# Kernel optimization log

Hardware: AMD Instinct MI355X
Metric: run time of the kernel (lower is better)

The kernel has to match this reference:

```python
import jax, jax.numpy as jnp
import numpy as np
from functools import partial

N = 10  # n_qubits (static)


def _rx(state, w, theta, n):
    # state: [B, 2^n] complex64; RX(theta) on wire w (wire 0 = most significant)
    B = state.shape[0]
    st = state.reshape(B, 2 ** w, 2, 2 ** (n - 1 - w))
    half = jnp.asarray(theta, state.real.dtype) * 0.5
    c = jnp.cos(half).reshape(-1, 1, 1)
    s = jnp.sin(half).reshape(-1, 1, 1)
    s0, s1 = st[:, :, 0], st[:, :, 1]
    n0 = c * s0 - 1j * s * s1
    n1 = -1j * s * s0 + c * s1
    return jnp.stack([n0, n1], axis=2).reshape(B, 2 ** n)


def _cnot(state, control, target, n):
    B = state.shape[0]
    a, bb = (control, target) if control < target else (target, control)
    st = state.reshape(B, 2 ** a, 2, 2 ** (bb - a - 1), 2, 2 ** (n - 1 - bb))
    if control == a:
        # control is axis 2, target axis 4: flip target where control==1
        c1 = jnp.flip(st[:, :, 1], axis=3)
        st = jnp.stack([st[:, :, 0], c1], axis=2)
    else:
        # control is axis 4, target axis 2: flip axis-2 slice where control==1
        c1 = jnp.flip(st[:, :, :, :, 1], axis=1)
        st = jnp.stack([st[:, :, :, :, 0], c1], axis=4)
    return st.reshape(B, 2 ** n)


def _expect_z(state, n):
    B = state.shape[0]
    probs = jnp.abs(state) ** 2  # [B, 2^n]
    es = []
    for w in range(n):
        p = probs.reshape(B, 2 ** w, 2, 2 ** (n - 1 - w))
        es.append(p[:, :, 0].sum((1, 2)) - p[:, :, 1].sum((1, 2)))
    return jnp.stack(es, axis=1)  # [B, n]


def _qlayer(x, theta, n):
    # x: [B, n] encoder angles; theta: [n] trainable RX angles
    B = x.shape[0]
    state = jnp.zeros((B, 2 ** n), jnp.complex64).at[:, 0].set(1.0)
    for w in range(n):
        state = _rx(state, w, x[:, w], n)
    for w in range(n):
        state = _rx(state, w, theta[w], n)
    for w in range(n - 1):
        state = _cnot(state, w, w + 1, n)
    state = _cnot(state, n - 1, 0, n)
    return _expect_z(state, n)


def setup_inputs() -> dict:
    key = jax.random.key(0)
    k1, k2, k3, k4 = jax.random.split(key, 4)
    T, B, D, H = 64, 256, 246, N
    inputs = jax.random.normal(k1, (T, B, D), jnp.float32)
    fan_in = D + H
    W = jax.random.normal(k2, (4, N, fan_in), jnp.float32) / np.sqrt(fan_in)
    b = jax.random.normal(k3, (4, N), jnp.float32) * 0.01
    thetas = jax.random.normal(k4, (4, N), jnp.float32)
    return {"inputs": inputs, "W": W, "b": b, "thetas": thetas}


def reference(inputs, W, b, thetas):
    T, B, D = inputs.shape
    H = thetas.shape[-1]
    qlayer4 = jax.vmap(partial(_qlayer, n=N))  # over the 4 gates

    def step(carry, x_t):
        hx, cx = carry
        comb = jnp.concatenate([x_t, hx], axis=1)          # [B, D+H]
        z = jnp.einsum('bi,goi->gbo', comb, W) + b[:, None, :]  # [4, B, n]
        gates = qlayer4(z, thetas)                          # [4, B, n]
        f = jax.nn.sigmoid(gates[0])
        i = jax.nn.sigmoid(gates[1])
        g = jnp.tanh(gates[2])
        o = jax.nn.sigmoid(gates[3])
        cx = f * cx + i * g
        hx = o * jnp.tanh(cx)
        return (hx, cx), hx

    hx0 = jnp.zeros((B, H), inputs.dtype)
    cx0 = jnp.zeros((B, H), inputs.dtype)
    (hx, cx), outputs = jax.lax.scan(step, (hx0, cx0), inputs)
    return outputs, hx, cx
```

## Files before the change

kernel.cpp:

```cpp
#include <hip/hip_runtime.h>
#include <hip/hip_bf16.h>

#define D_IN   246
#define NW     10
#define NG     4
#define NOUT   40
#define FANIN  256
#define BATCH  256
#define TSTEPS 64
#define XP     248
#define WP_ELEMS (NG * D_IN * 16)

__global__ __launch_bounds__(256) void k_wt(const float* __restrict__ W,
                                            float* __restrict__ Wp) {
    int e = blockIdx.x * 256 + threadIdx.x;
    if (e >= WP_ELEMS) return;
    int o = e & 15;
    int i = (e >> 4) % D_IN;
    int g = e / (16 * D_IN);
    float v = (o < NW) ? W[(g * NW + o) * FANIN + i] : 0.f;
    Wp[e] = v;
}

__global__ __launch_bounds__(256) void k_zx(
    const float* __restrict__ x,
    const float* __restrict__ Wp,
    const float* __restrict__ bias,
    const float* __restrict__ theta,
    float* __restrict__ zxT)
{
    const int t   = blockIdx.x;
    const int bq  = blockIdx.y;
    const int tid = threadIdx.x;
    const int lane = tid & 63;
    const int g = __builtin_amdgcn_readfirstlane(tid >> 6);

    __shared__ float xl[64 * XP];

    const float* xsrc = x + ((size_t)t * BATCH + bq * 64) * D_IN;
    for (int k = tid; k < 64 * 123; k += 256) {
        int row = k / 123;
        int j   = k - row * 123;
        float2 v = *reinterpret_cast<const float2*>(xsrc + row * D_IN + 2 * j);
        *reinterpret_cast<float2*>(xl + row * XP + 2 * j) = v;
    }
    __syncthreads();

    float acc[NW];
#pragma unroll
    for (int o = 0; o < NW; ++o)
        acc[o] = bias[g * NW + o] + theta[g * NW + o];

    const float* wg = Wp + g * D_IN * 16;
    const float* xr = xl + lane * XP;

#pragma unroll 1
    for (int i = 0; i < 244; i += 4) {
        float4 xv = *reinterpret_cast<const float4*>(xr + i);
        const float xs[4] = {xv.x, xv.y, xv.z, xv.w};
#pragma unroll
        for (int k2 = 0; k2 < 4; ++k2) {
#pragma unroll
            for (int o = 0; o < NW; ++o)
                acc[o] += xs[k2] * wg[(i + k2) * 16 + o];
        }
    }
    {
        float2 xv = *reinterpret_cast<const float2*>(xr + 244);
#pragma unroll
        for (int o = 0; o < NW; ++o) {
            acc[o] += xv.x * wg[244 * 16 + o];
            acc[o] += xv.y * wg[245 * 16 + o];
        }
    }

    const int b = bq * 64 + lane;
    float* zo = zxT + ((size_t)b * TSTEPS + t) * NOUT + g * NW;
#pragma unroll
    for (int o = 0; o < NW; ++o) zo[o] = acc[o];
}

template <int CTRL>
__device__ __forceinline__ float dpp_shr_mul(float p) {
    int up = __builtin_amdgcn_update_dpp(__float_as_int(1.0f), __float_as_int(p),
                                         CTRL, 0xF, 0xF, false);
    return p * __int_as_float(up);
}

__global__ __launch_bounds__(64) void k_scan(
    const float* __restrict__ zxT,
    const float* __restrict__ W,
    float* __restrict__ out,
    float* __restrict__ hxout,
    float* __restrict__ cxout)
{
    const int b    = blockIdx.x;
    const int lane = threadIdx.x;
    const int r    = lane >> 4;
    const int o    = lane & 15;
    const bool act = (o < NW);
    const int oc   = act ? o : 0;

    __shared__ float zl[TSTEPS * NOUT];

    {
        const float4* src4 = reinterpret_cast<const float4*>(zxT + (size_t)b * TSTEPS * NOUT);
        float4* dst4 = reinterpret_cast<float4*>(zl);
#pragma unroll
        for (int q = 0; q < 10; ++q) dst4[q * 64 + lane] = src4[q * 64 + lane];
    }

    float wh[NW];
#pragma unroll
    for (int j = 0; j < NW; ++j)
        wh[j] = W[(r * NW + oc) * FANIN + D_IN + j];

    __syncthreads();

    float hx_s[NW];
#pragma unroll
    for (int j = 0; j < NW; ++j) hx_s[j] = 0.f;

    float cx = 0.f, hv = 0.f;
    const int cidx = r * NW + oc;
    float zc = act ? zl[cidx] : 0.f;

    for (int t = 0; t < TSTEPS; ++t) {
        float zn = (act && t < TSTEPS - 1) ? zl[(t + 1) * NOUT + cidx] : 0.f;

        float z = zc;
#pragma unroll
        for (int j = 0; j < NW; ++j) z += hx_s[j] * wh[j];

        float cv = act ? __cosf(z) : 1.0f;

        float p = cv;
        p = dpp_shr_mul<0x111>(p);
        p = dpp_shr_mul<0x112>(p);
        p = dpp_shr_mul<0x114>(p);
        p = dpp_shr_mul<0x118>(p);

        float a   = (r == 2) ? p + p : p;
        float sg  = __fdividef(1.f, 1.f + __expf(-a));
        float val = (r == 2) ? 2.f * sg - 1.f : sg;

        float v1 = __shfl(val, 16 + o);
        float v2 = __shfl(val, 32 + o);
        float v3 = __shfl(val, 48 + o);

        cx = val * cx + v1 * v2;
        float e2 = __expf(cx + cx);
        float th = 1.f - __fdividef(2.f, e2 + 1.f);
        hv = v3 * th;

        if (r == 0 && act) out[((size_t)t * BATCH + b) * NW + o] = hv;

#pragma unroll
        for (int j = 0; j < NW; ++j)
            hx_s[j] = __int_as_float(__builtin_amdgcn_readlane(__float_as_int(hv), j));

        zc = zn;
    }

    if (r == 0 && act) {
        hxout[b * NW + o] = hv;
        cxout[b * NW + o] = cx;
    }
}

extern "C" void kernel_launch(void* const* d_in, const int* in_sizes, int n_in,
                              void* d_out, int out_size, void* d_ws, size_t ws_size,
                              hipStream_t stream) {
    const float* x     = (const float*)d_in[0];
    const float* W     = (const float*)d_in[1];
    const float* bias  = (const float*)d_in[2];
    const float* theta = (const float*)d_in[3];

    float* out   = (float*)d_out;
    float* hxout = out + (size_t)TSTEPS * BATCH * NW;
    float* cxout = hxout + (size_t)BATCH * NW;

    float* Wp  = (float*)d_ws;
    float* zxT = Wp + WP_ELEMS;

    k_wt<<<(WP_ELEMS + 255) / 256, 256, 0, stream>>>(W, Wp);
    dim3 g1(TSTEPS, 4);
    k_zx<<<g1, 256, 0, stream>>>(x, Wp, bias, theta, zxT);
    k_scan<<<BATCH, 64, 0, stream>>>(zxT, W, out, hxout, cxout);
}
```

Before: 126.2 us.

## Split zx projection K-dimension across two waves and streamline scan step

The input-projection kernel now uses 512 threads, with each gate split into two half-K waves that reduce through shared memory, and it writes its outputs as float2 stores. The scan loop drops the active-lane predicates, splits the hidden dot product into two FMA chains, and replaces the gate-gathering shuffles with XOR-pattern ds_bpermute plus lane-dependent selects so every lane holds all four gate values. The aim is more parallelism in the projection and a shorter serial dependency chain per timestep. The cost is an extra barrier and shared-memory reduction, and unpadded shared rows (stride 246) that may cause bank conflicts.

```diff
diff --git a/kernel.cpp b/kernel.cpp
--- a/kernel.cpp
+++ b/kernel.cpp
@@ -8,7 +8,6 @@
 #define FANIN  256
 #define BATCH  256
 #define TSTEPS 64
-#define XP     248
 #define WP_ELEMS (NG * D_IN * 16)
 
 __global__ __launch_bounds__(256) void k_wt(const float* __restrict__ W,
@@ -22,62 +21,69 @@
     Wp[e] = v;
 }
 
-__global__ __launch_bounds__(256) void k_zx(
+__global__ __launch_bounds__(512) void k_zx(
     const float* __restrict__ x,
     const float* __restrict__ Wp,
     const float* __restrict__ bias,
     const float* __restrict__ theta,
     float* __restrict__ zxT)
 {
-    const int t   = blockIdx.x;
-    const int bq  = blockIdx.y;
-    const int tid = threadIdx.x;
+    const int t    = blockIdx.x;
+    const int bq   = blockIdx.y;
+    const int tid  = threadIdx.x;
     const int lane = tid & 63;
-    const int g = __builtin_amdgcn_readfirstlane(tid >> 6);
-
-    __shared__ float xl[64 * XP];
+    const int wv   = __builtin_amdgcn_readfirstlane(tid >> 6);
+    const int g    = wv & 3;
+    const int kh   = wv >> 2;
+
+    __shared__ float xl[64 * D_IN];
+    __shared__ float pr[NG][64][NW];
 
     const float* xsrc = x + ((size_t)t * BATCH + bq * 64) * D_IN;
-    for (int k = tid; k < 64 * 123; k += 256) {
+    for (int k = tid; k < 64 * 123; k += 512) {
         int row = k / 123;
         int j   = k - row * 123;
         float2 v = *reinterpret_cast<const float2*>(xsrc + row * D_IN + 2 * j);
-        *reinterpret_cast<float2*>(xl + row * XP + 2 * j) = v;
+        *reinterpret_cast<float2*>(xl + row * D_IN + 2 * j) = v;
     }
     __syncthreads();
 
+    const int khbase = kh ? 124 : 0;
+    const int npairs = kh ? 61 : 62;
+
     float acc[NW];
 #pragma unroll
-    for (int o = 0; o < NW; ++o)
-        acc[o] = bias[g * NW + o] + theta[g * NW + o];
-
-    const float* wg = Wp + g * D_IN * 16;
-    const float* xr = xl + lane * XP;
-
-#pragma unroll 1
-    for (int i = 0; i < 244; i += 4) {
-        float4 xv = *reinterpret_cast<const float4*>(xr + i);
-        const float xs[4] = {xv.x, xv.y, xv.z, xv.w};
-#pragma unroll
-        for (int k2 = 0; k2 < 4; ++k2) {
-#pragma unroll
-            for (int o = 0; o < NW; ++o)
-                acc[o] += xs[k2] * wg[(i + k2) * 16 + o];
+    for (int o = 0; o < NW; ++o) acc[o] = 0.f;
+
+    const float* wg = Wp + (g * D_IN + khbase) * 16;
+    const float* xr = xl + lane * D_IN + khbase;
+
+#pragma unroll 2
+    for (int ii = 0; ii < npairs; ++ii) {
+        float2 xv = *reinterpret_cast<const float2*>(xr + 2 * ii);
+#pragma unroll
+        for (int o = 0; o < NW; ++o) {
+            acc[o] += xv.x * wg[(2 * ii)     * 16 + o];
+            acc[o] += xv.y * wg[(2 * ii + 1) * 16 + o];
         }
     }
-    {
-        float2 xv = *reinterpret_cast<const float2*>(xr + 244);
-#pragma unroll
-        for (int o = 0; o < NW; ++o) {
-            acc[o] += xv.x * wg[244 * 16 + o];
-            acc[o] += xv.y * wg[245 * 16 + o];
-        }
-    }
-
-    const int b = bq * 64 + lane;
-    float* zo = zxT + ((size_t)b * TSTEPS + t) * NOUT + g * NW;
-#pragma unroll
-    for (int o = 0; o < NW; ++o) zo[o] = acc[o];
+
+    if (kh == 1) {
+#pragma unroll
+        for (int o = 0; o < NW; ++o) pr[g][lane][o] = acc[o];
+    }
+    __syncthreads();
+
+    if (kh == 0) {
+#pragma unroll
+        for (int o = 0; o < NW; ++o)
+            acc[o] += pr[g][lane][o] + bias[g * NW + o] + theta[g * NW + o];
+        const int b = bq * 64 + lane;
+        float* zo = zxT + ((size_t)b * TSTEPS + t) * NOUT + g * NW;
+#pragma unroll
+        for (int q = 0; q < 5; ++q)
+            *reinterpret_cast<float2*>(zo + 2 * q) = make_float2(acc[2 * q], acc[2 * q + 1]);
+    }
 }
 
 template <int CTRL>
@@ -115,6 +121,15 @@
     for (int j = 0; j < NW; ++j)
         wh[j] = W[(r * NW + oc) * FANIN + D_IN + j];
 
+    const float am = (r == 2) ? 2.f : 1.f;
+    const float vm = (r == 2) ? 2.f : 1.f;
+    const float vc = (r == 2) ? -1.f : 0.f;
+    const int idx1 = (lane ^ 16) << 2;
+    const int idx2 = (lane ^ 32) << 2;
+    const int idx3 = (lane ^ 48) << 2;
+    const bool q1 = (r & 1) != 0;
+    const bool q2 = (r & 2) != 0;
+
     __syncthreads();
 
     float hx_s[NW];
@@ -126,13 +141,17 @@
     float zc = act ? zl[cidx] : 0.f;
 
     for (int t = 0; t < TSTEPS; ++t) {
-        float zn = (act && t < TSTEPS - 1) ? zl[(t + 1) * NOUT + cidx] : 0.f;
-
-        float z = zc;
-#pragma unroll
-        for (int j = 0; j < NW; ++j) z += hx_s[j] * wh[j];
-
-        float cv = act ? __cosf(z) : 1.0f;
+        float zn = zl[(((t + 1) & 63) * NOUT) + cidx];
+
+        float s0 = zc, s1 = 0.f;
+#pragma unroll
+        for (int j = 0; j < 5; ++j) {
+            s0 = fmaf(hx_s[2 * j],     wh[2 * j],     s0);
+            s1 = fmaf(hx_s[2 * j + 1], wh[2 * j + 1], s1);
+        }
+        float z = s0 + s1;
+
+        float cv = __cosf(z);
 
         float p = cv;
         p = dpp_shr_mul<0x111>(p);
@@ -140,18 +159,24 @@
         p = dpp_shr_mul<0x114>(p);
         p = dpp_shr_mul<0x118>(p);
 
-        float a   = (r == 2) ? p + p : p;
-        float sg  = __fdividef(1.f, 1.f + __expf(-a));
-        float val = (r == 2) ? 2.f * sg - 1.f : sg;
-
-        float v1 = __shfl(val, 16 + o);
-        float v2 = __shfl(val, 32 + o);
-        float v3 = __shfl(val, 48 + o);
-
-        cx = val * cx + v1 * v2;
+        float e  = __expf(-(p * am));
+        float sg = __fdividef(1.f, 1.f + e);
+        float val = fmaf(sg, vm, vc);
+
+        int vi = __float_as_int(val);
+        float a1 = __int_as_float(__builtin_amdgcn_ds_bpermute(idx1, vi));
+        float a2 = __int_as_float(__builtin_amdgcn_ds_bpermute(idx2, vi));
+        float a3 = __int_as_float(__builtin_amdgcn_ds_bpermute(idx3, vi));
+
+        float fv = q2 ? (q1 ? a3 : a2) : (q1 ? a1 : val);
+        float iv = q2 ? (q1 ? a2 : a3) : (q1 ? val : a1);
+        float gv = q2 ? (q1 ? a1 : val) : (q1 ? a3 : a2);
+        float ov = q2 ? (q1 ? val : a1) : (q1 ? a2 : a3);
+
+        cx = fmaf(fv, cx, iv * gv);
         float e2 = __expf(cx + cx);
-        float th = 1.f - __fdividef(2.f, e2 + 1.f);
-        hv = v3 * th;
+        float th = 1.f - __fdividef(2.f, 1.f + e2);
+        hv = ov * th;
 
         if (r == 0 && act) out[((size_t)t * BATCH + b) * NW + o] = hv;
 
@@ -185,6 +210,6 @@
 
     k_wt<<<(WP_ELEMS + 255) / 256, 256, 0, stream>>>(W, Wp);
     dim3 g1(TSTEPS, 4);
-    k_zx<<<g1, 256, 0, stream>>>(x, Wp, bias, theta, zxT);
+    k_zx<<<g1, 512, 0, stream>>>(x, Wp, bias, theta, zxT);
     k_scan<<<BATCH, 64, 0, stream>>>(zxT, W, out, hxout, cxout);
 }
```

After: 103.0 us. -18.4%, faster.
